# Performance work log

Hardware: AMD Instinct MI355X
Metric: run time of the kernel (lower is better)

The kernel has to match this reference:

```python
import jax, jax.numpy as jnp
import numpy as np

B, S, D, H = 2, 2048, 2048, 16
HD = D // H


def setup_inputs() -> dict:
    key = jax.random.key(0)
    kx, = jax.random.split(key, 1)
    return {
        "x": jax.random.normal(kx, (B, S, D), dtype=jnp.float32),
        "q_mask": jnp.ones((D, D), dtype=jnp.float32),
        "k_mask": jnp.ones((D, D), dtype=jnp.float32),
        "v_mask": jnp.ones((D, D), dtype=jnp.float32),
        "out_mask": jnp.ones((D, D), dtype=jnp.float32),
        "head_mask": jnp.ones((H,), dtype=jnp.float32),
        "attention_mask": jnp.ones((B, S), dtype=jnp.float32),
        "shared_weight": jnp.float32(1.0),
    }


def reference(x, q_mask, k_mask, v_mask, out_mask, head_mask, attention_mask, shared_weight):
    b, s, d = x.shape
    scale = jnp.float32(HD) ** -0.5

    def shared_linear(inp, mask):
        # F.linear(x, mask * shared_weight): out = inp @ (mask*sw).T
        return jnp.einsum("bsd,ed->bse", inp, mask * shared_weight)

    q = shared_linear(x, q_mask).reshape(b, s, H, HD).transpose(0, 2, 1, 3)  # [B,H,S,HD]
    k = shared_linear(x, k_mask).reshape(b, s, H, HD).transpose(0, 2, 1, 3)
    v = shared_linear(x, v_mask).reshape(b, s, H, HD).transpose(0, 2, 1, 3)

    hm = head_mask.reshape(1, H, 1, 1)
    q, k, v = q * hm, k * hm, v * hm

    scores = jnp.einsum("bhqd,bhkd->bhqk", q, k) * scale  # [B,H,S,S]

    # causal mask: upper triangle (j > i) -> -inf
    causal = jnp.triu(jnp.ones((s, s), dtype=bool), k=1)
    scores = jnp.where(causal, -jnp.inf, scores)

    # additive attention mask: (1 - m) * -10000, broadcast [B,1,1,S]
    scores = scores + (1.0 - attention_mask)[:, None, None, :] * -10000.0

    attn = jax.nn.softmax(scores, axis=-1)  # dropout is identity in eval / p=0

    out = jnp.einsum("bhqk,bhkd->bhqd", attn, v)          # [B,H,S,HD]
    out = out.transpose(0, 2, 1, 3).reshape(b, s, d)       # [B,S,D]
    return shared_linear(out, out_mask)
```

## Files before the change

### kernel.cpp

```cpp
#include <hip/hip_runtime.h>

#define B_  2
#define S_  2048
#define D_  2048
#define H_  16
#define HD_ 128

typedef __bf16 bf16;
typedef __bf16 bf16x4 __attribute__((ext_vector_type(4)));
typedef __bf16 bf16x8 __attribute__((ext_vector_type(8)));
typedef float  f32x4  __attribute__((ext_vector_type(4)));

__device__ __forceinline__ void gld_lds16(const void* g, void* l) {
    __builtin_amdgcn_global_load_lds(
        (const __attribute__((address_space(1))) unsigned int*)g,
        (__attribute__((address_space(3))) unsigned int*)l, 16, 0, 0);
}

__global__ __launch_bounds__(256)
void precast_kernel(const float* __restrict__ x, bf16* __restrict__ xh,
                    bf16* __restrict__ xl) {
    int i = (blockIdx.x * 256 + threadIdx.x) * 8;
    float4 a = *(const float4*)(x + i);
    float4 b = *(const float4*)(x + i + 4);
    float av[8] = {a.x, a.y, a.z, a.w, b.x, b.y, b.z, b.w};
    bf16x8 h8, l8;
#pragma unroll
    for (int e = 0; e < 8; e++) {
        bf16 hv = (bf16)av[e];
        h8[e] = hv;
        l8[e] = (bf16)(av[e] - (float)hv);
    }
    *(bf16x8*)(xh + i) = h8;
    *(bf16x8*)(xl + i) = l8;
}

__global__ __launch_bounds__(256)
void transpose_v(const bf16* __restrict__ vp, bf16* __restrict__ vt) {
    const int bh = blockIdx.x >> 5;
    const int s0 = (blockIdx.x & 31) * 64;
    const int t = threadIdx.x;
    __shared__ bf16 tile[128 * 72];
    const bf16* src = vp + (size_t)bh * S_ * HD_;
    bf16* dst = vt + (size_t)bh * HD_ * S_;
    {
        int r = t >> 2;
        int g = (t & 3) * 4;
#pragma unroll
        for (int w = 0; w < 4; w++) {
            bf16x8 v8 = *(const bf16x8*)&src[(size_t)(s0 + r) * HD_ + (g + w) * 8];
#pragma unroll
            for (int e = 0; e < 8; e++) tile[((g + w) * 8 + e) * 72 + r] = v8[e];
        }
    }
    __syncthreads();
    {
        int d = t >> 1;
        int sg0 = (t & 1) * 4;
#pragma unroll
        for (int w = 0; w < 4; w++) {
            int sg = sg0 + w;
            *(bf16x8*)&dst[(size_t)d * S_ + s0 + sg * 8] =
                *(const bf16x8*)&tile[d * 72 + sg * 8];
        }
    }
}

#define BK 64

template<int MODE>
__global__ __launch_bounds__(256, 3)
void gemm_nt(const bf16* __restrict__ Ah_g, const bf16* __restrict__ Al_g,
             const float* __restrict__ B0, const float* __restrict__ B1,
             const float* __restrict__ B2,
             const float* __restrict__ swp, const float* __restrict__ hm,
             bf16* __restrict__ qh_, bf16* __restrict__ ql_,
             bf16* __restrict__ kh_, bf16* __restrict__ kl_,
             bf16* __restrict__ vp_, float* __restrict__ Cf) {
    const int K = D_;
    __shared__ bf16 Ah[128 * 64];
    __shared__ bf16 Al[128 * 64];
    __shared__ bf16 Bs[128 * 64];
    const int t = threadIdx.x;
    const int wave = t >> 6, lane = t & 63;
    const int wr = wave >> 1, wc = wave & 1;
    const int m0 = blockIdx.y * 128, n0 = blockIdx.x * 128;
    const int lrow = lane & 15, lquad = lane >> 4;
    const float sw = swp[0];

    const int which = (MODE == 0) ? (n0 >> 11) : 0;
    const bool split = (MODE == 0) && (which < 2);

    const float* Bp;
    if (MODE == 0) {
        Bp = (which == 0) ? B0 : ((which == 1) ? B1 : B2);
        Bp += (size_t)(n0 & (D_ - 1)) * K;
    } else {
        Bp = B0 + (size_t)n0 * K;
    }

    const int srow8 = lane >> 3;
    const int sgrp  = lane & 7;
    const int g0 = (lquad)     ^ (lrow & 7);
    const int g1 = (lquad + 4) ^ (lrow & 7);

    f32x4 acc[4][4];
#pragma unroll
    for (int i = 0; i < 4; i++)
#pragma unroll
        for (int j = 0; j < 4; j++) acc[i][j] = (f32x4){0.f, 0.f, 0.f, 0.f};

    for (int k0 = 0; k0 < K; k0 += BK) {
#pragma unroll
        for (int p = 0; p < 4; p++) {
            int r = wave * 32 + p * 8 + srow8;
            int gcol = (sgrp ^ (r & 7)) * 8;
            gld_lds16(Ah_g + (size_t)(m0 + r) * K + k0 + gcol,
                      &Ah[(wave * 32 + p * 8) * 64]);
            if (split)
                gld_lds16(Al_g + (size_t)(m0 + r) * K + k0 + gcol,
                          &Al[(wave * 32 + p * 8) * 64]);
        }
#pragma unroll
        for (int p = 0; p < 4; p++) {
            int r = p * 32 + (t >> 3);
            int gcol = (sgrp ^ (r & 7)) * 8;
            const float* bp = Bp + (size_t)r * K + k0 + gcol;
            float4 blo = *(const float4*)bp;
            float4 bhi = *(const float4*)(bp + 4);
            bf16x8 b8;
            b8[0] = (bf16)(blo.x * sw); b8[1] = (bf16)(blo.y * sw);
            b8[2] = (bf16)(blo.z * sw); b8[3] = (bf16)(blo.w * sw);
            b8[4] = (bf16)(bhi.x * sw); b8[5] = (bf16)(bhi.y * sw);
            b8[6] = (bf16)(bhi.z * sw); b8[7] = (bf16)(bhi.w * sw);
            *(bf16x8*)&Bs[r * 64 + sgrp * 8] = b8;
        }
        __syncthreads();

#pragma unroll
        for (int kk = 0; kk < 2; kk++) {
            const int gA = kk ? g1 : g0;
            bf16x8 afh[4], afl[4], bfr[4];
#pragma unroll
            for (int i = 0; i < 4; i++) {
                int row = wr * 64 + i * 16 + lrow;
                afh[i] = *(const bf16x8*)&Ah[row * 64 + gA * 8];
                if (split) afl[i] = *(const bf16x8*)&Al[row * 64 + gA * 8];
            }
#pragma unroll
            for (int j = 0; j < 4; j++) {
                int row = wc * 64 + j * 16 + lrow;
                bfr[j] = *(const bf16x8*)&Bs[row * 64 + gA * 8];
            }
#pragma unroll
            for (int i = 0; i < 4; i++)
#pragma unroll
                for (int j = 0; j < 4; j++) {
                    acc[i][j] = __builtin_amdgcn_mfma_f32_16x16x32_bf16(
                        afh[i], bfr[j], acc[i][j], 0, 0, 0);
                    if (split)
                        acc[i][j] = __builtin_amdgcn_mfma_f32_16x16x32_bf16(
                            afl[i], bfr[j], acc[i][j], 0, 0, 0);
                }
        }
        __syncthreads();
    }

#pragma unroll
    for (int i = 0; i < 4; i++) {
#pragma unroll
        for (int j = 0; j < 4; j++) {
#pragma unroll
            for (int r = 0; r < 4; r++) {
                int m = m0 + wr * 64 + i * 16 + lquad * 4 + r;
                int n = n0 + wc * 64 + j * 16 + lrow;
                float v = acc[i][j][r];
                if (MODE == 0) {
                    int e = n & (D_ - 1);
                    int h = e >> 7, hd = e & (HD_ - 1);
                    int b = m >> 11, s = m & (S_ - 1);
                    v *= hm[h];
                    size_t idx = (((size_t)b * H_ + h) * S_ + s) * HD_ + hd;
                    if (which == 2) {
                        vp_[idx] = (bf16)v;
                    } else {
                        bf16 hv = (bf16)v;
                        bf16 lv = (bf16)(v - (float)hv);
                        if (which == 0) { qh_[idx] = hv; ql_[idx] = lv; }
                        else            { kh_[idx] = hv; kl_[idx] = lv; }
                    }
                } else {
                    Cf[(size_t)m * D_ + n] = v;
                }
            }
        }
    }
}

#define SPLD 72

__global__ __launch_bounds__(256, 2)
void attn_kernel(const bf16* __restrict__ qh_, const bf16* __restrict__ ql_,
                 const bf16* __restrict__ kh_, const bf16* __restrict__ kl_,
                 const bf16* __restrict__ vt_, const float* __restrict__ am,
                 bf16* __restrict__ outp) {
    const int bh = blockIdx.x & 31;
    const int qblk = 31 - (blockIdx.x >> 5);
    const int b = bh >> 4, h = bh & 15;
    const int i0 = qblk * 64;
    const int t = threadIdx.x, wave = t >> 6, lane = t & 63;
    const int lrow = lane & 15, quad = lane >> 4;

    __shared__ bf16 skh[64 * 128];
    __shared__ bf16 skl[64 * 128];
    __shared__ bf16 svt[128 * 64];
    __shared__ bf16 sp[4][16 * SPLD];

    const size_t kbase = (size_t)bh * S_ * HD_;
    const size_t vbase = (size_t)bh * HD_ * S_;

    int krr[4], kcc[4], ldk[4];
#pragma unroll
    for (int p = 0; p < 4; p++) {
        int r = wave * 16 + p * 4 + (lane >> 4);
        krr[p] = r;
        kcc[p] = ((lane & 15) ^ (r & 7)) * 8;
        ldk[p] = r * 128 + (lane & 15) * 8;
    }
    int vdd[4], vcc[4], ldv[4];
#pragma unroll
    for (int p = 0; p < 4; p++) {
        int d = wave * 32 + p * 8 + (lane >> 3);
        vdd[p] = d;
        vcc[p] = ((lane & 7) ^ (d & 7)) * 8;
        ldv[p] = d * 64 + (lane & 7) * 8;
    }

    const int qrow = i0 + wave * 16 + lrow;
    bf16x8 qhf[4], qlf[4];
#pragma unroll
    for (int c = 0; c < 4; c++) {
        qhf[c] = *(const bf16x8*)&qh_[kbase + (size_t)qrow * HD_ + c * 32 + quad * 8];
        qlf[c] = *(const bf16x8*)&ql_[kbase + (size_t)qrow * HD_ + c * 32 + quad * 8];
    }

    bf16x8 ones8;
#pragma unroll
    for (int e = 0; e < 8; e++) ones8[e] = (bf16)1.0f;

    float m_i[4];
    f32x4 O[8], Ol;
#pragma unroll
    for (int r = 0; r < 4; r++) m_i[r] = -INFINITY;
#pragma unroll
    for (int n2 = 0; n2 < 8; n2++) O[n2] = (f32x4){0.f, 0.f, 0.f, 0.f};
    Ol = (f32x4){0.f, 0.f, 0.f, 0.f};

    const float scale2 = 0.08838834764831845f * 1.44269504088896f;
    const int nch = (i0 >> 6) + 1;

    bf16x8 pkh[4], pkl[4], pvt[4];
#pragma unroll
    for (int p = 0; p < 4; p++) {
        pkh[p] = *(const bf16x8*)&kh_[kbase + (size_t)krr[p] * HD_ + kcc[p]];
        pkl[p] = *(const bf16x8*)&kl_[kbase + (size_t)krr[p] * HD_ + kcc[p]];
        pvt[p] = *(const bf16x8*)&vt_[vbase + (size_t)vdd[p] * S_ + vcc[p]];
    }

    for (int c = 0; c < nch; c++) {
        const int j0 = c * 64;
        __syncthreads();
#pragma unroll
        for (int p = 0; p < 4; p++) {
            *(bf16x8*)&skh[ldk[p]] = pkh[p];
            *(bf16x8*)&skl[ldk[p]] = pkl[p];
            *(bf16x8*)&svt[ldv[p]] = pvt[p];
        }
        __syncthreads();
        if (c + 1 < nch) {
            const int j0n = j0 + 64;
#pragma unroll
            for (int p = 0; p < 4; p++) {
                pkh[p] = *(const bf16x8*)&kh_[kbase + (size_t)(j0n + krr[p]) * HD_ + kcc[p]];
                pkl[p] = *(const bf16x8*)&kl_[kbase + (size_t)(j0n + krr[p]) * HD_ + kcc[p]];
                pvt[p] = *(const bf16x8*)&vt_[vbase + (size_t)vdd[p] * S_ + j0n + vcc[p]];
            }
        }

        float amadd[4];
#pragma unroll
        for (int nt = 0; nt < 4; nt++)
            amadd[nt] = (1.0f - am[b * S_ + j0 + nt * 16 + lrow]) * -14426.950408f;

        f32x4 s4[4];
#pragma unroll
        for (int nt = 0; nt < 4; nt++) s4[nt] = (f32x4){0.f, 0.f, 0.f, 0.f};
#pragma unroll
        for (int cg = 0; cg < 4; cg++) {
#pragma unroll
            for (int nt = 0; nt < 4; nt++) {
                int ka = (nt * 16 + lrow) * 128 + (((cg * 4 + quad) ^ (lrow & 7)) * 8);
                bf16x8 kb8 = *(const bf16x8*)&skh[ka];
                bf16x8 lb8 = *(const bf16x8*)&skl[ka];
                s4[nt] = __builtin_amdgcn_mfma_f32_16x16x32_bf16(qhf[cg], kb8, s4[nt], 0, 0, 0);
                s4[nt] = __builtin_amdgcn_mfma_f32_16x16x32_bf16(qhf[cg], lb8, s4[nt], 0, 0, 0);
                s4[nt] = __builtin_amdgcn_mfma_f32_16x16x32_bf16(qlf[cg], kb8, s4[nt], 0, 0, 0);
            }
        }

        const bool diag = (j0 == i0);
#pragma unroll
        for (int r = 0; r < 4; r++) {
            const int rrow = wave * 16 + quad * 4 + r;
            float sv[4];
            float mx = -INFINITY;
#pragma unroll
            for (int nt = 0; nt < 4; nt++) {
                float xv = s4[nt][r] * scale2 + amadd[nt];
                if (diag && (nt * 16 + lrow) > rrow) xv = -INFINITY;
                sv[nt] = xv;
                mx = fmaxf(mx, xv);
            }
#pragma unroll
            for (int off = 1; off < 16; off <<= 1) mx = fmaxf(mx, __shfl_xor(mx, off));
            float mnew = fmaxf(m_i[r], mx);
            float alpha = exp2f(m_i[r] - mnew);
            m_i[r] = mnew;
            Ol[r] *= alpha;
#pragma unroll
            for (int n2 = 0; n2 < 8; n2++) O[n2][r] *= alpha;
#pragma unroll
            for (int nt = 0; nt < 4; nt++)
                sp[wave][(quad * 4 + r) * SPLD + nt * 16 + lrow] = (bf16)exp2f(sv[nt] - mnew);
        }
        __asm__ volatile("s_waitcnt lgkmcnt(0)" ::: "memory");

#pragma unroll
        for (int k2 = 0; k2 < 2; k2++) {
            bf16x8 pf = *(const bf16x8*)&sp[wave][lrow * SPLD + k2 * 32 + quad * 8];
            const int gp = ((quad + k2 * 4) ^ (lrow & 7)) * 8;
#pragma unroll
            for (int n2 = 0; n2 < 8; n2++) {
                bf16x8 vf8 = *(const bf16x8*)&svt[(n2 * 16 + lrow) * 64 + gp];
                O[n2] = __builtin_amdgcn_mfma_f32_16x16x32_bf16(pf, vf8, O[n2], 0, 0, 0);
            }
            Ol = __builtin_amdgcn_mfma_f32_16x16x32_bf16(pf, ones8, Ol, 0, 0, 0);
        }
    }

    float inv[4];
#pragma unroll
    for (int r = 0; r < 4; r++) inv[r] = 1.0f / Ol[r];
#pragma unroll
    for (int n2 = 0; n2 < 8; n2++)
#pragma unroll
        for (int r = 0; r < 4; r++) {
            int srow = i0 + wave * 16 + quad * 4 + r;
            outp[((size_t)(b * S_ + srow)) * D_ + h * HD_ + n2 * 16 + lrow] =
                (bf16)(O[n2][r] * inv[r]);
        }
}

extern "C" void kernel_launch(void* const* d_in, const int* in_sizes, int n_in,
                              void* d_out, int out_size, void* d_ws, size_t ws_size,
                              hipStream_t stream) {
    const float* x  = (const float*)d_in[0];
    const float* qm = (const float*)d_in[1];
    const float* km = (const float*)d_in[2];
    const float* vm = (const float*)d_in[3];
    const float* om = (const float*)d_in[4];
    const float* hm = (const float*)d_in[5];
    const float* am = (const float*)d_in[6];
    const float* sw = (const float*)d_in[7];
    float* out = (float*)d_out;

    const size_t P = (size_t)B_ * H_ * S_ * HD_ * sizeof(bf16);
    char* ws = (char*)d_ws;
    bf16* xh = (bf16*)(ws + 0 * P);
    bf16* xl = (bf16*)(ws + 1 * P);
    bf16* qh = (bf16*)(ws + 2 * P);
    bf16* ql = (bf16*)(ws + 3 * P);
    bf16* kh = (bf16*)(ws + 4 * P);
    bf16* kl = (bf16*)(ws + 5 * P);
    bf16* vp = (bf16*)d_out;
    bf16* vt = (bf16*)((char*)d_out + P);
    bf16* attn_out = (bf16*)(ws + 0 * P);

    precast_kernel<<<(B_ * S_ * D_) / (256 * 8), 256, 0, stream>>>(x, xh, xl);

    gemm_nt<0><<<dim3(48, 32), 256, 0, stream>>>(
        xh, xl, qm, km, vm, sw, hm, qh, ql, kh, kl, vp, nullptr);

    transpose_v<<<1024, 256, 0, stream>>>(vp, vt);

    attn_kernel<<<1024, 256, 0, stream>>>(qh, ql, kh, kl, vt, am, attn_out);

    gemm_nt<1><<<dim3(16, 32), 256, 0, stream>>>(
        attn_out, nullptr, om, nullptr, nullptr, sw, hm,
        nullptr, nullptr, nullptr, nullptr, nullptr, out);
}
```

Before: 495.7 us.

## Load K tiles via global_load_lds, read V directly from global, raise occupancy

```diff
diff --git a/kernel.cpp b/kernel.cpp
--- a/kernel.cpp
+++ b/kernel.cpp
@@ -197,9 +197,7 @@
     }
 }
 
-#define SPLD 72
-
-__global__ __launch_bounds__(256, 2)
+__global__ __launch_bounds__(256, 4)
 void attn_kernel(const bf16* __restrict__ qh_, const bf16* __restrict__ ql_,
                  const bf16* __restrict__ kh_, const bf16* __restrict__ kl_,
                  const bf16* __restrict__ vt_, const float* __restrict__ am,
@@ -213,28 +211,10 @@
 
     __shared__ bf16 skh[64 * 128];
     __shared__ bf16 skl[64 * 128];
-    __shared__ bf16 svt[128 * 64];
-    __shared__ bf16 sp[4][16 * SPLD];
+    __shared__ bf16 spm[4][16 * 64];
 
     const size_t kbase = (size_t)bh * S_ * HD_;
     const size_t vbase = (size_t)bh * HD_ * S_;
-
-    int krr[4], kcc[4], ldk[4];
-#pragma unroll
-    for (int p = 0; p < 4; p++) {
-        int r = wave * 16 + p * 4 + (lane >> 4);
-        krr[p] = r;
-        kcc[p] = ((lane & 15) ^ (r & 7)) * 8;
-        ldk[p] = r * 128 + (lane & 15) * 8;
-    }
-    int vdd[4], vcc[4], ldv[4];
-#pragma unroll
-    for (int p = 0; p < 4; p++) {
-        int d = wave * 32 + p * 8 + (lane >> 3);
-        vdd[p] = d;
-        vcc[p] = ((lane & 7) ^ (d & 7)) * 8;
-        ldv[p] = d * 64 + (lane & 7) * 8;
-    }
 
     const int qrow = i0 + wave * 16 + lrow;
     bf16x8 qhf[4], qlf[4];
@@ -259,33 +239,18 @@
     const float scale2 = 0.08838834764831845f * 1.44269504088896f;
     const int nch = (i0 >> 6) + 1;
 
-    bf16x8 pkh[4], pkl[4], pvt[4];
-#pragma unroll
-    for (int p = 0; p < 4; p++) {
-        pkh[p] = *(const bf16x8*)&kh_[kbase + (size_t)krr[p] * HD_ + kcc[p]];
-        pkl[p] = *(const bf16x8*)&kl_[kbase + (size_t)krr[p] * HD_ + kcc[p]];
-        pvt[p] = *(const bf16x8*)&vt_[vbase + (size_t)vdd[p] * S_ + vcc[p]];
-    }
-
     for (int c = 0; c < nch; c++) {
         const int j0 = c * 64;
         __syncthreads();
 #pragma unroll
         for (int p = 0; p < 4; p++) {
-            *(bf16x8*)&skh[ldk[p]] = pkh[p];
-            *(bf16x8*)&skl[ldk[p]] = pkl[p];
-            *(bf16x8*)&svt[ldv[p]] = pvt[p];
+            int rb = wave * 16 + p * 4;
+            int r  = rb + (lane >> 4);
+            int gl = ((lane & 15) ^ (r & 7)) * 8;
+            gld_lds16(kh_ + kbase + (size_t)(j0 + r) * HD_ + gl, &skh[rb * 128]);
+            gld_lds16(kl_ + kbase + (size_t)(j0 + r) * HD_ + gl, &skl[rb * 128]);
         }
         __syncthreads();
-        if (c + 1 < nch) {
-            const int j0n = j0 + 64;
-#pragma unroll
-            for (int p = 0; p < 4; p++) {
-                pkh[p] = *(const bf16x8*)&kh_[kbase + (size_t)(j0n + krr[p]) * HD_ + kcc[p]];
-                pkl[p] = *(const bf16x8*)&kl_[kbase + (size_t)(j0n + krr[p]) * HD_ + kcc[p]];
-                pvt[p] = *(const bf16x8*)&vt_[vbase + (size_t)vdd[p] * S_ + j0n + vcc[p]];
-            }
-        }
 
         float amadd[4];
 #pragma unroll
@@ -329,21 +294,27 @@
             Ol[r] *= alpha;
 #pragma unroll
             for (int n2 = 0; n2 < 8; n2++) O[n2][r] *= alpha;
-#pragma unroll
-            for (int nt = 0; nt < 4; nt++)
-                sp[wave][(quad * 4 + r) * SPLD + nt * 16 + lrow] = (bf16)exp2f(sv[nt] - mnew);
+            const int rl = quad * 4 + r;
+#pragma unroll
+            for (int nt = 0; nt < 4; nt++) {
+                int phys = ((nt * 2 + (lrow >> 3)) ^ (rl & 7));
+                spm[wave][rl * 64 + phys * 8 + (lrow & 7)] = (bf16)exp2f(sv[nt] - mnew);
+            }
         }
         __asm__ volatile("s_waitcnt lgkmcnt(0)" ::: "memory");
 
 #pragma unroll
         for (int k2 = 0; k2 < 2; k2++) {
-            bf16x8 pf = *(const bf16x8*)&sp[wave][lrow * SPLD + k2 * 32 + quad * 8];
-            const int gp = ((quad + k2 * 4) ^ (lrow & 7)) * 8;
-#pragma unroll
-            for (int n2 = 0; n2 < 8; n2++) {
-                bf16x8 vf8 = *(const bf16x8*)&svt[(n2 * 16 + lrow) * 64 + gp];
-                O[n2] = __builtin_amdgcn_mfma_f32_16x16x32_bf16(pf, vf8, O[n2], 0, 0, 0);
-            }
+            int pg = ((k2 * 4 + quad) ^ (lrow & 7)) * 8;
+            bf16x8 pf = *(const bf16x8*)&spm[wave][lrow * 64 + pg];
+            bf16x8 vf[8];
+#pragma unroll
+            for (int n2 = 0; n2 < 8; n2++)
+                vf[n2] = *(const bf16x8*)&vt_[vbase + (size_t)(n2 * 16 + lrow) * S_ +
+                                              j0 + k2 * 32 + quad * 8];
+#pragma unroll
+            for (int n2 = 0; n2 < 8; n2++)
+                O[n2] = __builtin_amdgcn_mfma_f32_16x16x32_bf16(pf, vf[n2], O[n2], 0, 0, 0);
             Ol = __builtin_amdgcn_mfma_f32_16x16x32_bf16(pf, ones8, Ol, 0, 0, 0);
         }
     }
```

Measured after the change: 768.2 us. 1.55x slower.
